# Kernel tuning notes

Hardware: AMD Instinct MI355X
Metric: run time of the kernel (lower is better)

Reference implementation:

```python
import jax, jax.numpy as jnp
import numpy as np

# ---- architecture constants (from init_kwargs / arch_args) ----
IN_BITS, IN_FRAC, BITS_PER_STREAM = 8, 4, 2
N_STREAMS = IN_BITS // BITS_PER_STREAM          # 4
W_BITS, BITS_PER_SLICE = 8, 2
N_SLICES = W_BITS // BITS_PER_SLICE             # 4
ADC_BITS = 5
ADC_MAX = 2.0 ** ADC_BITS - 1.0                 # 31
SUBARRAY_SIZE = 128
IC, OC, K, STRIDE, PAD = 64, 64, 3, 1, 1
F_TOTAL = IC * K * K                            # 576 unfolded features
N_SUB = (F_TOTAL + SUBARRAY_SIZE - 1) // SUBARRAY_SIZE  # 5 subarrays
CHUNK = -(-F_TOTAL // N_SUB)                    # 116, matches torch.chunk sizes


def bit_stream(x):
    """VectorizedInputBitStreaming.forward: fixed-point quantize + two's complement + bit-serial split."""
    int_bits = IN_BITS - IN_FRAC - 1
    max_val = 2.0 ** int_bits - 2.0 ** (-IN_FRAC)
    q = jnp.round(jnp.clip(x, -(2.0 ** int_bits), max_val) * (2 ** IN_FRAC)).astype(jnp.int32)
    q = jnp.where(q < 0, (1 << IN_BITS) + q, q)  # two's complement encode
    shifts = jnp.arange(0, IN_BITS, BITS_PER_STREAM, dtype=jnp.int32)
    return ((q[..., None] >> shifts) & ((1 << BITS_PER_STREAM) - 1)).astype(jnp.float32)


def bit_slice(w):
    """VectorizedWeightBitSlicing.forward: pos/neg split, normalize by max abs, integer bit-slice."""
    wp = jnp.maximum(w, 0.0)
    wn = jnp.maximum(-w, 0.0)
    max_abs = jnp.maximum(wp.max(), wn.max())
    max_abs = jnp.where(max_abs > 0, max_abs, 1.0)
    mv = 2 ** W_BITS - 1
    pi = jnp.round(wp / max_abs * mv).astype(jnp.int32)
    ni = jnp.round(wn / max_abs * mv).astype(jnp.int32)
    shifts = jnp.arange(0, W_BITS, BITS_PER_SLICE, dtype=jnp.int32)
    mask = (1 << BITS_PER_SLICE) - 1
    pos = ((pi[..., None] >> shifts) & mask).astype(jnp.float32)
    neg = ((ni[..., None] >> shifts) & mask).astype(jnp.float32)
    return pos, neg, max_abs


def adc(x):
    """Nbit_ADC simulated: uniform round + clip to [0, 2^adc_bits - 1]."""
    return jnp.clip(jnp.round(x), 0.0, ADC_MAX)


def _forward(inputs, weight):
    # unfold -> (B, IC*K*K, H', W') with (c, kh, kw)-major feature ordering like F.unfold
    patches = jax.lax.conv_general_dilated_patches(
        inputs, (K, K), (STRIDE, STRIDE), [(PAD, PAD), (PAD, PAD)])
    B, F, H, W = patches.shape
    P = H * W
    patches = patches.reshape(B, F, P)

    streams = bit_stream(patches)                     # (B, F, P, S)
    pos_sl, neg_sl, norm = bit_slice(weight)
    pos_m = pos_sl.reshape(OC, F, N_SLICES)           # (O, F, T)
    neg_m = neg_sl.reshape(OC, F, N_SLICES)

    # zero-pad feature dim to N_SUB*CHUNK and reshape into subarray chunks
    pad = N_SUB * CHUNK - F
    streams = jnp.pad(streams, ((0, 0), (0, pad), (0, 0), (0, 0))).reshape(B, N_SUB, CHUNK, P, N_STREAMS)
    pos_m = jnp.pad(pos_m, ((0, 0), (0, pad), (0, 0))).reshape(OC, N_SUB, CHUNK, N_SLICES)
    neg_m = jnp.pad(neg_m, ((0, 0), (0, pad), (0, 0))).reshape(OC, N_SUB, CHUNK, N_SLICES)

    # per-subarray analog MAC: (c, b, o, p, s, t)
    pos_r = jnp.einsum('bcfps,ocft->cbopst', streams, pos_m)
    neg_r = jnp.einsum('bcfps,ocft->cbopst', streams, neg_m)

    # ADC quantize, then weight by 2^(stream*bits) * 2^(slice*bits), sum over s,t and subarrays c
    scale = (2.0 ** (jnp.arange(N_STREAMS) * BITS_PER_STREAM))[:, None] * \
            (2.0 ** (jnp.arange(N_SLICES) * BITS_PER_SLICE))[None, :]
    diff = jnp.einsum('cbopst,st->bop', adc(pos_r) - adc(neg_r), scale)

    out = diff * norm / (2.0 ** IN_BITS - 1.0)
    return out.reshape(B, OC, H, W), jnp.float32(0.0)


def setup_inputs() -> dict:
    key = jax.random.key(0)
    k1, k2 = jax.random.split(key)
    inputs = jax.random.normal(k1, (4, IC, 32, 32), dtype=jnp.float32)
    # kaiming_normal_-like init
    weight = jax.random.normal(k2, (OC, IC, K, K), dtype=jnp.float32) * (2.0 / (IC * K * K)) ** 0.5
    return {"inputs": inputs, "weight": weight}


def reference(inputs, weight):
    return _forward(inputs, weight)
```

## Files before the change

### kernel.cpp

```cpp
#include <hip/hip_runtime.h>
#include <stdint.h>


typedef int v4i __attribute__((ext_vector_type(4)));
typedef unsigned int v4u __attribute__((ext_vector_type(4)));

#define BROW  656
#define BROWD 164

__device__ __forceinline__ v4i bits2(v4u w, int s) {
  v4u r = (w >> (unsigned)(2 * s)) & 0x03030303u;
  return (v4i)r;
}

__global__ __launch_bounds__(512, 4) void k_fused(
    const float* __restrict__ in, const float* __restrict__ w,
    float* __restrict__ out)
{
  __shared__ __align__(16) unsigned char Al[32 * BROW];
  __shared__ __align__(16) unsigned char Bl[32 * BROW];
  __shared__ float s_part[8];

  int tid = threadIdx.x;
  int bid = blockIdx.x;
  if (bid == 0 && tid == 0) out[262144] = 0.0f;

  int mtile = bid >> 2;
  int otile = bid & 3;

  float amax = 0.0f;
  {
    const float4* w4 = (const float4*)w;
    #pragma unroll 6
    for (int i = 0; i < 18; ++i) {
      float4 v = w4[i * 512 + tid];
      amax = fmaxf(amax, fmaxf(fmaxf(fabsf(v.x), fabsf(v.y)),
                               fmaxf(fabsf(v.z), fabsf(v.w))));
    }
  }

  {
    int row  = tid >> 4;
    int slot = tid & 15;
    int c, dw;
    if (slot < 12) { c = (slot * 11) >> 5; dw = 29 + slot - c * 3; }
    else           { c = 4;                dw = slot + 16; }
    ((unsigned int*)Bl)[row * BROWD + c * 32 + dw] = 0u;
  }

  {
    int b = mtile >> 5;
    int yrow = mtile & 31;
    #pragma unroll 2
    for (int i = 0; i < 10; ++i) {
      int d = i * 512 + tid;
      unsigned int m_l = ((unsigned)d * 52429u) >> 23;
      int kw = d - (int)m_l * 160;
      unsigned int pack = 0;
      #pragma unroll
      for (int q = 0; q < 4; ++q) {
        int k = kw * 4 + q;
        int c = k >> 7, j = k & 127;
        int csize = (c == 4) ? 112 : 116;
        unsigned int bv = 0;
        if (j < csize) {
          unsigned int f  = c * 116 + j;
          unsigned int ic = (f * 7282u) >> 16;
          unsigned int r9 = f - ic * 9u;
          unsigned int dy = (r9 * 11u) >> 5;
          unsigned int dx = r9 - dy * 3u;
          int iy = yrow + (int)dy - 1, ix = (int)m_l + (int)dx - 1;
          if (iy >= 0 && iy < 32 && ix >= 0 && ix < 32) {
            float xv = in[((b * 64 + (int)ic) * 32 + iy) * 32 + ix];
            xv = fminf(fmaxf(xv, -8.0f), 7.9375f);
            bv = (unsigned int)((int)rintf(xv * 16.0f) & 255);
          }
        }
        pack |= bv << (8 * q);
      }
      ((unsigned int*)Al)[m_l * BROWD + kw] = pack;
    }
  }

  #pragma unroll
  for (int off = 32; off > 0; off >>= 1)
    amax = fmaxf(amax, __shfl_down(amax, off, 64));
  if ((tid & 63) == 0) s_part[tid >> 6] = amax;
  __syncthreads();

  float norm = s_part[0];
  #pragma unroll
  for (int i = 1; i < 8; ++i) norm = fmaxf(norm, s_part[i]);
  if (!(norm > 0.0f)) norm = 1.0f;
  float sc = 255.0f / norm;

  #pragma unroll
  for (int i = 0; i < 5; ++i) {
    int idx = i * 512 + tid;
    if (idx < 2304) {
      unsigned int o_l = ((unsigned)idx * 1821u) >> 18;
      int g = idx - (int)o_l * 144;
      int c, jg;
      if (g < 116) { c = (g * 565) >> 14; jg = (g - c * 29) * 4; }
      else         { c = 4;               jg = (g - 116) * 4; }
      int f = c * 116 + jg;
      float4 wv = *(const float4*)(w + (otile * 16 + (int)o_l) * 576 + f);
      float vv[4] = {wv.x, wv.y, wv.z, wv.w};
      unsigned int pd = 0, nd = 0;
      #pragma unroll
      for (int q = 0; q < 4; ++q) {
        unsigned int pb = (unsigned int)(int)rintf(fmaxf(vv[q], 0.0f) * sc);
        unsigned int nb = (unsigned int)(int)rintf(fmaxf(-vv[q], 0.0f) * sc);
        pd |= pb << (8 * q);
        nd |= nb << (8 * q);
      }
      int dwo = c * 32 + (jg >> 2);
      ((unsigned int*)Bl)[(int)o_l * BROWD + dwo]        = pd;
      ((unsigned int*)Bl)[(16 + (int)o_l) * BROWD + dwo] = nd;
    }
  }
  __syncthreads();

  int lane = tid & 63, wave = tid >> 6;
  int s = wave & 3, msub = wave >> 2;
  int r16 = lane & 15, kgrp = lane >> 4;

  const unsigned char* ap = Al + (msub * 16 + r16) * BROW + kgrp * 16;
  const unsigned char* bp = Bl + r16 * BROW + kgrp * 16;
  const unsigned char* bn = Bl + (16 + r16) * BROW + kgrp * 16;

  v4i outacc = {0, 0, 0, 0};

  #pragma unroll
  for (int c = 0; c < 5; ++c) {
    v4u a0 = *(const v4u*)(ap + c * 128);
    v4u a1 = *(const v4u*)(ap + c * 128 + 64);
    v4u p0 = *(const v4u*)(bp + c * 128);
    v4u p1 = *(const v4u*)(bp + c * 128 + 64);
    v4u n0 = *(const v4u*)(bn + c * 128);
    v4u n1 = *(const v4u*)(bn + c * 128 + 64);

    v4i as0 = bits2(a0, s), as1 = bits2(a1, s);

    #pragma unroll
    for (int t = 0; t < 4; ++t) {
      v4i z = {0, 0, 0, 0};
      v4i pacc = __builtin_amdgcn_mfma_i32_16x16x64_i8(bits2(p0, t), as0, z, 0, 0, 0);
      pacc     = __builtin_amdgcn_mfma_i32_16x16x64_i8(bits2(p1, t), as1, pacc, 0, 0, 0);
      v4i nacc = __builtin_amdgcn_mfma_i32_16x16x64_i8(bits2(n0, t), as0, z, 0, 0, 0);
      nacc     = __builtin_amdgcn_mfma_i32_16x16x64_i8(bits2(n1, t), as1, nacc, 0, 0, 0);
      int sh = 2 * (s + t);
      #pragma unroll
      for (int r = 0; r < 4; ++r) {
        int dd = (pacc[r] < 31 ? pacc[r] : 31) - (nacc[r] < 31 ? nacc[r] : 31);
        outacc[r] += dd << sh;
      }
    }
  }

  __syncthreads();
  v4i* red = (v4i*)Al;
  red[wave * 64 + lane] = outacc;
  __syncthreads();

  if (s == 0) {
    v4i acc = red[(msub * 4 + 0) * 64 + lane];
    #pragma unroll
    for (int ss = 1; ss < 4; ++ss)
      acc += red[(msub * 4 + ss) * 64 + lane];
    float fsc = norm / 255.0f;
    int pg = mtile * 32 + msub * 16 + r16;
    int b = pg >> 10, p = pg & 1023;
    int oc = otile * 16 + kgrp * 4;
    #pragma unroll
    for (int r = 0; r < 4; ++r)
      out[(b * 64 + oc + r) * 1024 + p] = (float)acc[r] * fsc;
  }
}

extern "C" void kernel_launch(void* const* d_in, const int* in_sizes, int n_in,
                              void* d_out, int out_size, void* d_ws, size_t ws_size,
                              hipStream_t stream) {
  const float* inp = (const float*)d_in[0];
  const float* wgt = (const float*)d_in[1];
  float* out = (float*)d_out;
  (void)d_ws; (void)ws_size;
  k_fused<<<512, 512, 0, stream>>>(inp, wgt, out);
}
```

Baseline: 88.96 us.

## Split into prep kernel for quantized patches/weight max and smaller main GEMM kernel

Moves input im2col quantization and weight abs-max reduction into a separate prep kernel that writes packed int8 patches to workspace. The main kernel then reads the packed patches directly from global memory, keeping only the weight slices in LDS. It also halves the block size and tile to 16 pixels, doubling the grid. This removes the redundant global weight max scan that every block did and the per-block patch staging, at the cost of an extra launch and a global round-trip for the patches.

```diff
diff --git a/kernel.cpp b/kernel.cpp
--- a/kernel.cpp
+++ b/kernel.cpp
@@ -5,127 +5,132 @@
 typedef int v4i __attribute__((ext_vector_type(4)));
 typedef unsigned int v4u __attribute__((ext_vector_type(4)));
 
+#define WS_PART   0
+#define WS_AQ     1024
+
 #define BROW  656
 #define BROWD 164
+
+__global__ __launch_bounds__(256) void k_prep(
+    const float* __restrict__ in, const float* __restrict__ w,
+    unsigned char* __restrict__ Aq, float* __restrict__ part,
+    float* __restrict__ out_scalar)
+{
+  int bid = blockIdx.x, tid = threadIdx.x;
+  if (bid == 0 && tid == 0) out_scalar[0] = 0.0f;
+  if (bid < 2560) {
+    unsigned int widx = bid * 256 + tid;
+    unsigned int m  = ((widx >> 5) * 52429u) >> 18;
+    unsigned int kw = widx - m * 160;
+    int b = m >> 10, p = m & 1023;
+    int y = p >> 5, x = p & 31;
+    unsigned int pack = 0;
+    #pragma unroll
+    for (int i = 0; i < 4; ++i) {
+      unsigned int k = kw * 4 + i;
+      unsigned int c = k >> 7;
+      unsigned int j = k & 127;
+      unsigned int csize = (c == 4) ? 112 : 116;
+      unsigned int bv = 0;
+      if (j < csize) {
+        unsigned int f  = c * 116 + j;
+        unsigned int ic = (f * 7282u) >> 16;
+        unsigned int r9 = f - ic * 9;
+        unsigned int dy = (r9 * 11u) >> 5;
+        unsigned int dx = r9 - dy * 3;
+        int iy = y + (int)dy - 1, ix = x + (int)dx - 1;
+        if (iy >= 0 && iy < 32 && ix >= 0 && ix < 32) {
+          float xv = in[((b * 64 + (int)ic) * 32 + iy) * 32 + ix];
+          xv = fminf(fmaxf(xv, -8.0f), 7.9375f);
+          bv = (unsigned int)((int)rintf(xv * 16.0f) & 255);
+        }
+      }
+      pack |= bv << (8 * i);
+    }
+    ((unsigned int*)Aq)[widx] = pack;
+  } else {
+    int t = (bid - 2560) * 256 + tid;
+    const float4 wv = ((const float4*)w)[t];
+    float a = fmaxf(fmaxf(fabsf(wv.x), fabsf(wv.y)),
+                    fmaxf(fabsf(wv.z), fabsf(wv.w)));
+    #pragma unroll
+    for (int off = 32; off > 0; off >>= 1)
+      a = fmaxf(a, __shfl_down(a, off, 64));
+    if ((tid & 63) == 0)
+      part[(bid - 2560) * 4 + (tid >> 6)] = a;
+  }
+}
 
 __device__ __forceinline__ v4i bits2(v4u w, int s) {
   v4u r = (w >> (unsigned)(2 * s)) & 0x03030303u;
   return (v4i)r;
 }
 
-__global__ __launch_bounds__(512, 4) void k_fused(
-    const float* __restrict__ in, const float* __restrict__ w,
-    float* __restrict__ out)
+__global__ __launch_bounds__(256, 4) void k_main(
+    const unsigned char* __restrict__ Aq, const float* __restrict__ w,
+    const float* __restrict__ part, float* __restrict__ out)
 {
-  __shared__ __align__(16) unsigned char Al[32 * BROW];
   __shared__ __align__(16) unsigned char Bl[32 * BROW];
-  __shared__ float s_part[8];
+  __shared__ __align__(16) v4i red[4 * 64];
+  __shared__ float s_norm;
 
   int tid = threadIdx.x;
   int bid = blockIdx.x;
-  if (bid == 0 && tid == 0) out[262144] = 0.0f;
-
   int mtile = bid >> 2;
   int otile = bid & 3;
 
-  float amax = 0.0f;
-  {
-    const float4* w4 = (const float4*)w;
-    #pragma unroll 6
-    for (int i = 0; i < 18; ++i) {
-      float4 v = w4[i * 512 + tid];
-      amax = fmaxf(amax, fmaxf(fmaxf(fabsf(v.x), fabsf(v.y)),
-                               fmaxf(fabsf(v.z), fabsf(v.w))));
-    }
-  }
-
-  {
-    int row  = tid >> 4;
-    int slot = tid & 15;
+  #pragma unroll
+  for (int i = 0; i < 2; ++i) {
+    int idx = i * 256 + tid;
+    int row = idx >> 4, slot = idx & 15;
     int c, dw;
     if (slot < 12) { c = (slot * 11) >> 5; dw = 29 + slot - c * 3; }
     else           { c = 4;                dw = slot + 16; }
     ((unsigned int*)Bl)[row * BROWD + c * 32 + dw] = 0u;
   }
-
-  {
-    int b = mtile >> 5;
-    int yrow = mtile & 31;
-    #pragma unroll 2
-    for (int i = 0; i < 10; ++i) {
-      int d = i * 512 + tid;
-      unsigned int m_l = ((unsigned)d * 52429u) >> 23;
-      int kw = d - (int)m_l * 160;
-      unsigned int pack = 0;
-      #pragma unroll
-      for (int q = 0; q < 4; ++q) {
-        int k = kw * 4 + q;
-        int c = k >> 7, j = k & 127;
-        int csize = (c == 4) ? 112 : 116;
-        unsigned int bv = 0;
-        if (j < csize) {
-          unsigned int f  = c * 116 + j;
-          unsigned int ic = (f * 7282u) >> 16;
-          unsigned int r9 = f - ic * 9u;
-          unsigned int dy = (r9 * 11u) >> 5;
-          unsigned int dx = r9 - dy * 3u;
-          int iy = yrow + (int)dy - 1, ix = (int)m_l + (int)dx - 1;
-          if (iy >= 0 && iy < 32 && ix >= 0 && ix < 32) {
-            float xv = in[((b * 64 + (int)ic) * 32 + iy) * 32 + ix];
-            xv = fminf(fmaxf(xv, -8.0f), 7.9375f);
-            bv = (unsigned int)((int)rintf(xv * 16.0f) & 255);
-          }
-        }
-        pack |= bv << (8 * q);
-      }
-      ((unsigned int*)Al)[m_l * BROWD + kw] = pack;
-    }
-  }
-
-  #pragma unroll
-  for (int off = 32; off > 0; off >>= 1)
-    amax = fmaxf(amax, __shfl_down(amax, off, 64));
-  if ((tid & 63) == 0) s_part[tid >> 6] = amax;
-  __syncthreads();
-
-  float norm = s_part[0];
-  #pragma unroll
-  for (int i = 1; i < 8; ++i) norm = fmaxf(norm, s_part[i]);
-  if (!(norm > 0.0f)) norm = 1.0f;
-  float sc = 255.0f / norm;
-
-  #pragma unroll
-  for (int i = 0; i < 5; ++i) {
-    int idx = i * 512 + tid;
-    if (idx < 2304) {
-      unsigned int o_l = ((unsigned)idx * 1821u) >> 18;
-      int g = idx - (int)o_l * 144;
-      int c, jg;
-      if (g < 116) { c = (g * 565) >> 14; jg = (g - c * 29) * 4; }
-      else         { c = 4;               jg = (g - 116) * 4; }
-      int f = c * 116 + jg;
-      float4 wv = *(const float4*)(w + (otile * 16 + (int)o_l) * 576 + f);
-      float vv[4] = {wv.x, wv.y, wv.z, wv.w};
-      unsigned int pd = 0, nd = 0;
-      #pragma unroll
-      for (int q = 0; q < 4; ++q) {
-        unsigned int pb = (unsigned int)(int)rintf(fmaxf(vv[q], 0.0f) * sc);
-        unsigned int nb = (unsigned int)(int)rintf(fmaxf(-vv[q], 0.0f) * sc);
-        pd |= pb << (8 * q);
-        nd |= nb << (8 * q);
-      }
-      int dwo = c * 32 + (jg >> 2);
-      ((unsigned int*)Bl)[(int)o_l * BROWD + dwo]        = pd;
-      ((unsigned int*)Bl)[(16 + (int)o_l) * BROWD + dwo] = nd;
-    }
+  if (tid < 64) {
+    float a = part[tid];
+    a = fmaxf(a, part[tid + 64]);
+    if (tid < 16) a = fmaxf(a, part[tid + 128]);
+    #pragma unroll
+    for (int off = 32; off > 0; off >>= 1)
+      a = fmaxf(a, __shfl_down(a, off, 64));
+    if (tid == 0) s_norm = (a > 0.0f) ? a : 1.0f;
   }
   __syncthreads();
 
-  int lane = tid & 63, wave = tid >> 6;
-  int s = wave & 3, msub = wave >> 2;
+  float norm = s_norm;
+  float sc = 255.0f / norm;
+
+  #pragma unroll 3
+  for (int i = 0; i < 9; ++i) {
+    int idx = i * 256 + tid;
+    unsigned int o_l = ((unsigned)idx * 1821u) >> 18;
+    int g = idx - (int)o_l * 144;
+    int c, jg;
+    if (g < 116) { c = (g * 565) >> 14; jg = (g - c * 29) * 4; }
+    else         { c = 4;               jg = (g - 116) * 4; }
+    int f = c * 116 + jg;
+    float4 wv = *(const float4*)(w + (otile * 16 + (int)o_l) * 576 + f);
+    float vv[4] = {wv.x, wv.y, wv.z, wv.w};
+    unsigned int pd = 0, nd = 0;
+    #pragma unroll
+    for (int q = 0; q < 4; ++q) {
+      unsigned int pb = (unsigned int)(int)rintf(fmaxf(vv[q], 0.0f) * sc);
+      unsigned int nb = (unsigned int)(int)rintf(fmaxf(-vv[q], 0.0f) * sc);
+      pd |= pb << (8 * q);
+      nd |= nb << (8 * q);
+    }
+    int dwo = c * 32 + (jg >> 2);
+    ((unsigned int*)Bl)[(int)o_l * BROWD + dwo]        = pd;
+    ((unsigned int*)Bl)[(16 + (int)o_l) * BROWD + dwo] = nd;
+  }
+  __syncthreads();
+
+  int lane = tid & 63, s = tid >> 6;
   int r16 = lane & 15, kgrp = lane >> 4;
 
-  const unsigned char* ap = Al + (msub * 16 + r16) * BROW + kgrp * 16;
+  const unsigned char* ap = Aq + (mtile * 16 + r16) * 640 + kgrp * 16;
   const unsigned char* bp = Bl + r16 * BROW + kgrp * 16;
   const unsigned char* bn = Bl + (16 + r16) * BROW + kgrp * 16;
 
@@ -158,18 +163,15 @@
     }
   }
 
+  red[s * 64 + lane] = outacc;
   __syncthreads();
-  v4i* red = (v4i*)Al;
-  red[wave * 64 + lane] = outacc;
-  __syncthreads();
-
   if (s == 0) {
-    v4i acc = red[(msub * 4 + 0) * 64 + lane];
+    v4i acc = red[lane];
     #pragma unroll
     for (int ss = 1; ss < 4; ++ss)
-      acc += red[(msub * 4 + ss) * 64 + lane];
+      acc += red[ss * 64 + lane];
     float fsc = norm / 255.0f;
-    int pg = mtile * 32 + msub * 16 + r16;
+    int pg = mtile * 16 + r16;
     int b = pg >> 10, p = pg & 1023;
     int oc = otile * 16 + kgrp * 4;
     #pragma unroll
@@ -184,6 +186,11 @@
   const float* inp = (const float*)d_in[0];
   const float* wgt = (const float*)d_in[1];
   float* out = (float*)d_out;
-  (void)d_ws; (void)ws_size;
-  k_fused<<<512, 512, 0, stream>>>(inp, wgt, out);
+  unsigned char* ws = (unsigned char*)d_ws;
+
+  float*         part = (float*)(ws + WS_PART);
+  unsigned char* Aq   = ws + WS_AQ;
+
+  k_prep<<<2596, 256, 0, stream>>>(inp, wgt, Aq, part, out + 262144);
+  k_main<<<1024, 256, 0, stream>>>(Aq, wgt, part, out);
 }
```

New measurement: 82.85 us. -6.9%, faster.
